# Optimization experiments

Measured on AMD Instinct MI355X. Metric: run time of the kernel, lower is better.

The kernel has to match this reference:

```python
import jax, jax.numpy as jnp
import numpy as np
import math

B, S, D = 4, 2048, 1024
NUM_HEADS = 16
HEAD_DIM = D // NUM_HEADS


def setup_inputs() -> dict:
    key = jax.random.key(0)
    ks = jax.random.split(key, 6)
    scale = 1.0 / math.sqrt(D)
    batch = jax.random.normal(ks[0], (B, S, D), dtype=jnp.float32)
    w_query = jax.random.normal(ks[1], (D, D), dtype=jnp.float32) * scale
    w_key = jax.random.normal(ks[2], (D, D), dtype=jnp.float32) * scale
    w_value = jax.random.normal(ks[3], (D, D), dtype=jnp.float32) * scale
    out_w = jax.random.normal(ks[4], (D, D), dtype=jnp.float32) * scale
    out_b = jax.random.normal(ks[5], (D,), dtype=jnp.float32) * 0.01
    return {"batch": batch, "w_query": w_query, "w_key": w_key,
            "w_value": w_value, "out_w": out_w, "out_b": out_b}


def reference(batch, w_query, w_key, w_value, out_w, out_b):
    b, s, _ = batch.shape
    # QKV projections (Linear with no bias): x @ W^T, here weights stored as [D,D] applied as x@W
    q = (batch @ w_query).reshape(b, s, NUM_HEADS, HEAD_DIM)
    k = (batch @ w_key).reshape(b, s, NUM_HEADS, HEAD_DIM)
    v = (batch @ w_value).reshape(b, s, NUM_HEADS, HEAD_DIM)
    # scores: [b, h, s, s]
    scores = jnp.einsum('bqhd,bkhd->bhqk', q, k)
    causal = jnp.tril(jnp.ones((s, s), dtype=bool))
    scores = jnp.where(causal, scores, -jnp.inf)
    # original divides by sqrt(head_dim) AFTER masking (-inf stays -inf)
    weights = jax.nn.softmax(scores / math.sqrt(HEAD_DIM), axis=-1)
    # dropout_percent = 0 -> identity
    out = jnp.einsum('bhqk,bkhd->bqhd', weights, v).reshape(b, s, D)
    return out @ out_w + out_b
```

## Files before the change

kernel.cpp:

```cpp
#include <hip/hip_runtime.h>
#include <hip/hip_bf16.h>

#define S_LEN 2048
#define D_DIM 1024
#define NHEAD 16
#define HDIM  64
#define BATCH 4
#define MROWS (BATCH*S_LEN)

typedef short bf16x8 __attribute__((ext_vector_type(8)));
typedef float f32x4  __attribute__((ext_vector_type(4)));
typedef float f32x16 __attribute__((ext_vector_type(16)));
typedef unsigned short u16;

#if __has_builtin(__builtin_amdgcn_exp2f)
#define EXP2(x) __builtin_amdgcn_exp2f(x)
#else
#define EXP2(x) __expf((x) * 0.6931471805599453f)
#endif

__device__ inline u16 f2bf(float f) {
  union { float f; unsigned u; } v; v.f = f;
  unsigned r = v.u + 0x7fff + ((v.u >> 16) & 1);
  return (u16)(r >> 16);
}

__device__ inline unsigned cvtpk(float lo, float hi_) {
  unsigned d;
  asm("v_cvt_pk_bf16_f32 %0, %1, %2" : "=v"(d) : "v"(lo), "v"(hi_));
  return d;
}

__device__ inline void perm32swap(unsigned& a, unsigned& b) {
  asm volatile("v_permlane32_swap_b32 %0, %1" : "+v"(a), "+v"(b));
}

__device__ inline void gload_lds16(const void* g, void* l) {
  __builtin_amdgcn_global_load_lds(
      (const __attribute__((address_space(1))) void*)g,
      (__attribute__((address_space(3))) void*)l, 16, 0, 0);
}

__global__ void cvt_x_kernel(const float* __restrict__ x, u16* __restrict__ xb, int n4) {
  int i = blockIdx.x * 256 + threadIdx.x;
  if (i >= n4) return;
  float4 v = reinterpret_cast<const float4*>(x)[i];
  ushort4 o;
  o.x = f2bf(v.x); o.y = f2bf(v.y); o.z = f2bf(v.z); o.w = f2bf(v.w);
  reinterpret_cast<ushort4*>(xb)[i] = o;
}

__global__ void transpose_w4_kernel(const float* __restrict__ wq, const float* __restrict__ wk,
                                    const float* __restrict__ wv, const float* __restrict__ wo,
                                    u16* __restrict__ wqkvT, u16* __restrict__ woT) {
  __shared__ float t[32][33];
  int z = blockIdx.z;
  const float* w = (z == 0) ? wq : (z == 1) ? wk : (z == 2) ? wv : wo;
  u16* wt = (z < 3) ? (wqkvT + (size_t)z * 1024 * 1024) : woT;
  int tx = threadIdx.x, ty = threadIdx.y;
  int n0 = blockIdx.x * 32, k0 = blockIdx.y * 32;
#pragma unroll
  for (int j = 0; j < 32; j += 8)
    t[ty + j][tx] = w[(size_t)(k0 + ty + j) * D_DIM + n0 + tx];
  __syncthreads();
#pragma unroll
  for (int j = 0; j < 32; j += 8)
    wt[(size_t)(n0 + ty + j) * D_DIM + k0 + tx] = f2bf(t[tx][ty + j]);
}

template <int EPI>
__global__ __launch_bounds__(256) void gemm_bt_kernel(
    const u16* __restrict__ A, const u16* __restrict__ Bt,
    void* __restrict__ Cv, u16* __restrict__ KP, u16* __restrict__ VP,
    const float* __restrict__ bias) {
  __shared__ u16 lA[128 * 32];
  __shared__ u16 lB[128 * 32];
  const int tid = threadIdx.x, wid = tid >> 6, lane = tid & 63;
  const int bm = blockIdx.y, bn = blockIdx.x;
  const int fr = lane & 15, fq = lane >> 4;
  const int r0 = wid * 32;
  const int srow = lane >> 2, scol = (lane & 3) * 8;
  const u16* gA = A + (size_t)(bm * 128 + r0 + srow) * 1024 + scol;
  const u16* gB = Bt + (size_t)(bn * 128 + r0 + srow) * 1024 + scol;
  u16* lA0 = &lA[r0 * 32];
  u16* lB0 = &lB[r0 * 32];

  f32x4 acc[4][4] = {};
  const int wm = (wid >> 1) * 64, wn = (wid & 1) * 64;

  for (int k0 = 0; k0 < 1024; k0 += 32) {
    gload_lds16(gA + k0,             lA0);
    gload_lds16(gA + k0 + 16 * 1024, lA0 + 16 * 32);
    gload_lds16(gB + k0,             lB0);
    gload_lds16(gB + k0 + 16 * 1024, lB0 + 16 * 32);
    __syncthreads();
    bf16x8 fa[4], fb[4];
#pragma unroll
    for (int i = 0; i < 4; i++) {
      fa[i] = *(const bf16x8*)&lA[(wm + i * 16 + fr) * 32 + fq * 8];
      fb[i] = *(const bf16x8*)&lB[(wn + i * 16 + fr) * 32 + fq * 8];
    }
#pragma unroll
    for (int i = 0; i < 4; i++)
#pragma unroll
      for (int j = 0; j < 4; j++)
        acc[i][j] = __builtin_amdgcn_mfma_f32_16x16x32_bf16(fa[i], fb[j], acc[i][j], 0, 0, 0);
    __syncthreads();
  }

  if (EPI == 1) {
#pragma unroll
    for (int i = 0; i < 4; i++)
#pragma unroll
      for (int j = 0; j < 4; j++)
#pragma unroll
        for (int r = 0; r < 4; r++) {
          int row = bm * 128 + wm + i * 16 + fq * 4 + r;
          int col = bn * 128 + wn + j * 16 + fr;
          ((float*)Cv)[(size_t)row * 1024 + col] = acc[i][j][r] + bias[col];
        }
    return;
  }

  const int col0 = bn * 128;
  if (col0 < 1024) {
#pragma unroll
    for (int i = 0; i < 4; i++)
#pragma unroll
      for (int j = 0; j < 4; j++)
#pragma unroll
        for (int r = 0; r < 4; r++) {
          int row = bm * 128 + wm + i * 16 + fq * 4 + r;
          int col = col0 + wn + j * 16 + fr;
          ((u16*)Cv)[(size_t)row * 1024 + col] = f2bf(acc[i][j][r]);
        }
  } else if (col0 < 2048) {
#pragma unroll
    for (int i = 0; i < 4; i++)
#pragma unroll
      for (int j = 0; j < 4; j++) {
        int col = col0 + wn + j * 16 + fr;
        int ck = col - 1024;
        int h = ck >> 6, d = ck & 63;
        int sfr = d >> 4, e = d & 7, hb = (d >> 3) & 1;
#pragma unroll
        for (int r = 0; r < 4; r++) {
          int row = bm * 128 + wm + i * 16 + fq * 4 + r;
          int b = row >> 11, sp = row & 2047;
          int bh = b * 16 + h, jt = sp >> 5;
          int lanep = (sp & 31) + 32 * hb;
          KP[((size_t)(bh * 64 + jt) * 4 + sfr) * 512 + lanep * 8 + e] = f2bf(acc[i][j][r]);
        }
      }
  } else {
#pragma unroll
    for (int i = 0; i < 4; i++)
#pragma unroll
      for (int j = 0; j < 4; j++) {
        int col = col0 + wn + j * 16 + fr;
        int cv = col - 2048;
        int h = cv >> 6, d = cv & 63;
        int R0 = bm * 128 + wm + i * 16 + fq * 4;
        int b = R0 >> 11, sp0 = R0 & 2047;
        int bh = b * 16 + h, jt = sp0 >> 5;
        int c = (d >> 5) * 2 + ((sp0 >> 4) & 1);
        int lanep = (d & 31) + 32 * ((sp0 >> 3) & 1);
        int e0 = sp0 & 7;
        ushort4 ov;
        ov.x = f2bf(acc[i][j][0]); ov.y = f2bf(acc[i][j][1]);
        ov.z = f2bf(acc[i][j][2]); ov.w = f2bf(acc[i][j][3]);
        *(ushort4*)(VP + ((size_t)(bh * 64 + jt) * 4 + c) * 512 + lanep * 8 + e0) = ov;
      }
  }
}

__global__ __launch_bounds__(256) void attn_kernel(
    const u16* __restrict__ Q, const u16* __restrict__ KP,
    const u16* __restrict__ VP, u16* __restrict__ O) {
  const int tid = threadIdx.x, wid = tid >> 6, lane = tid & 63;
  const int lq = lane & 31, hi = lane >> 5;
  int f = blockIdx.x;
  int xcd = f & 7, kk = f >> 3;
  int bh = xcd * 8 + (kk & 7);
  int qblk = 15 - (kk >> 3);
  int b = bh >> 4, h = bh & 15;
  int q0 = qblk * 128 + wid * 32;
  int q = q0 + lq;

  const u16* Qrow = Q + (size_t)(b * S_LEN + q) * D_DIM + h * HDIM;
  bf16x8 qf[4];
#pragma unroll
  for (int s = 0; s < 4; s++)
    qf[s] = *(const bf16x8*)(Qrow + s * 16 + hi * 8);

  const bf16x8* KPt = (const bf16x8*)KP + (size_t)bh * 64 * 4 * 64;
  const bf16x8* VPt = (const bf16x8*)VP + (size_t)bh * 64 * 4 * 64;

  f32x16 acc0 = {}, acc1 = {};
  float m = -3.0e38f, l = 0.f;
  const int nt = qblk * 4 + wid + 1;

  for (int t = 0; t < nt; ++t) {
    const int j0 = t * 32;
    const size_t fb = (size_t)t * 4 * 64 + lane;
    bf16x8 kf0 = KPt[fb], kf1 = KPt[fb + 64], kf2 = KPt[fb + 128], kf3 = KPt[fb + 192];
    bf16x8 vf00 = VPt[fb], vf01 = VPt[fb + 64], vf10 = VPt[fb + 128], vf11 = VPt[fb + 192];

    f32x16 sa = {};
    __builtin_amdgcn_s_setprio(1);
    sa = __builtin_amdgcn_mfma_f32_32x32x16_bf16(kf0, qf[0], sa, 0, 0, 0);
    sa = __builtin_amdgcn_mfma_f32_32x32x16_bf16(kf1, qf[1], sa, 0, 0, 0);
    sa = __builtin_amdgcn_mfma_f32_32x32x16_bf16(kf2, qf[2], sa, 0, 0, 0);
    sa = __builtin_amdgcn_mfma_f32_32x32x16_bf16(kf3, qf[3], sa, 0, 0, 0);
    __builtin_amdgcn_s_setprio(0);

    float p[16];
#pragma unroll
    for (int r = 0; r < 16; ++r) p[r] = sa[r] * 0.1803368801f;

    if (t == nt - 1) {
#pragma unroll
      for (int r = 0; r < 16; ++r) {
        int kidx = j0 + (r & 3) + 8 * (r >> 2) + 4 * hi;
        if (kidx > q) p[r] = -3.0e38f;
      }
    }

    float x8[8], x4[4], x2[2];
#pragma unroll
    for (int i = 0; i < 8; ++i) x8[i] = fmaxf(p[2 * i], p[2 * i + 1]);
#pragma unroll
    for (int i = 0; i < 4; ++i) x4[i] = fmaxf(x8[2 * i], x8[2 * i + 1]);
    x2[0] = fmaxf(x4[0], x4[1]); x2[1] = fmaxf(x4[2], x4[3]);
    float pm = fmaxf(x2[0], x2[1]);
    pm = fmaxf(pm, __shfl_xor(pm, 32));

    if (__any(pm > m + 11.5f)) {
      float mn = fmaxf(m, pm);
      float sc = EXP2(m - mn);
      l *= sc;
#pragma unroll
      for (int r = 0; r < 16; ++r) { acc0[r] *= sc; acc1[r] *= sc; }
      m = mn;
    }

    float rs = 0.f;
#pragma unroll
    for (int r = 0; r < 16; ++r) { p[r] = EXP2(p[r] - m); rs += p[r]; }
    rs += __shfl_xor(rs, 32);
    l += rs;

    unsigned c0 = cvtpk(p[0],  p[1]),  c1 = cvtpk(p[2],  p[3]);
    unsigned c2 = cvtpk(p[4],  p[5]),  c3 = cvtpk(p[6],  p[7]);
    unsigned c4 = cvtpk(p[8],  p[9]),  c5 = cvtpk(p[10], p[11]);
    unsigned c6 = cvtpk(p[12], p[13]), c7 = cvtpk(p[14], p[15]);
    perm32swap(c0, c2); perm32swap(c1, c3);
    perm32swap(c4, c6); perm32swap(c5, c7);
    union U4 { unsigned u[4]; bf16x8 v; } F0, F1;
    F0.u[0] = c0; F0.u[1] = c1; F0.u[2] = c2; F0.u[3] = c3;
    F1.u[0] = c4; F1.u[1] = c5; F1.u[2] = c6; F1.u[3] = c7;

    __builtin_amdgcn_s_setprio(1);
    acc0 = __builtin_amdgcn_mfma_f32_32x32x16_bf16(vf00, F0.v, acc0, 0, 0, 0);
    acc0 = __builtin_amdgcn_mfma_f32_32x32x16_bf16(vf01, F1.v, acc0, 0, 0, 0);
    acc1 = __builtin_amdgcn_mfma_f32_32x32x16_bf16(vf10, F0.v, acc1, 0, 0, 0);
    acc1 = __builtin_amdgcn_mfma_f32_32x32x16_bf16(vf11, F1.v, acc1, 0, 0, 0);
    __builtin_amdgcn_s_setprio(0);
  }

  float inv = 1.f / l;
  u16* Orow = O + (size_t)(b * S_LEN + q) * D_DIM + h * HDIM;
#pragma unroll
  for (int g = 0; g < 4; ++g) {
    ushort4 o4;
    o4.x = f2bf(acc0[g * 4 + 0] * inv);
    o4.y = f2bf(acc0[g * 4 + 1] * inv);
    o4.z = f2bf(acc0[g * 4 + 2] * inv);
    o4.w = f2bf(acc0[g * 4 + 3] * inv);
    *(ushort4*)(Orow + 8 * g + 4 * hi) = o4;
  }
#pragma unroll
  for (int g = 0; g < 4; ++g) {
    ushort4 o4;
    o4.x = f2bf(acc1[g * 4 + 0] * inv);
    o4.y = f2bf(acc1[g * 4 + 1] * inv);
    o4.z = f2bf(acc1[g * 4 + 2] * inv);
    o4.w = f2bf(acc1[g * 4 + 3] * inv);
    *(ushort4*)(Orow + 32 + 8 * g + 4 * hi) = o4;
  }
}

extern "C" void kernel_launch(void* const* d_in, const int* in_sizes, int n_in,
                              void* d_out, int out_size, void* d_ws, size_t ws_size,
                              hipStream_t stream) {
  const float* x  = (const float*)d_in[0];
  const float* wq = (const float*)d_in[1];
  const float* wk = (const float*)d_in[2];
  const float* wv = (const float*)d_in[3];
  const float* wo = (const float*)d_in[4];
  const float* ob = (const float*)d_in[5];
  float* out = (float*)d_out;

  char* ws = (char*)d_ws;
  u16* Xb    = (u16*)(ws);
  u16* Ab    = (u16*)(ws);
  u16* Qb    = (u16*)(ws + (size_t)16 * 1024 * 1024);
  u16* KPb   = (u16*)(ws + (size_t)32 * 1024 * 1024);
  u16* VPb   = (u16*)(ws + (size_t)48 * 1024 * 1024);
  u16* WqkvT = (u16*)(ws + (size_t)64 * 1024 * 1024);
  u16* WoT   = (u16*)(ws + (size_t)70 * 1024 * 1024);

  cvt_x_kernel<<<(MROWS * D_DIM / 4) / 256, 256, 0, stream>>>(x, Xb, MROWS * D_DIM / 4);

  transpose_w4_kernel<<<dim3(32, 32, 4), dim3(32, 8), 0, stream>>>(
      wq, wk, wv, wo, WqkvT, WoT);

  gemm_bt_kernel<0><<<dim3(24, 64), 256, 0, stream>>>(
      Xb, WqkvT, Qb, KPb, VPb, nullptr);

  attn_kernel<<<dim3(1024), 256, 0, stream>>>(Qb, KPb, VPb, Ab);

  gemm_bt_kernel<1><<<dim3(8, 64), 256, 0, stream>>>(
      Ab, WoT, out, nullptr, nullptr, ob);
}
```

Baseline: 177.6 us.

## Double-buffer LDS tiles in the projection GEMM to overlap loads with MFMA

The GEMM mainloop now keeps two LDS buffers for A and B. The global-to-LDS loads for the next K tile are issued before the MFMAs on the current tile, so memory latency can overlap with compute, and each iteration uses one barrier instead of two. The cost is twice the LDS per block, which may lower occupancy, and the loop is now fully unrolled. The manual s_waitcnt and s_barrier depend on the compiler not reordering the LDS reads.

```diff
diff --git a/kernel.cpp b/kernel.cpp
--- a/kernel.cpp
+++ b/kernel.cpp
@@ -18,6 +18,9 @@
 #else
 #define EXP2(x) __expf((x) * 0.6931471805599453f)
 #endif
+
+#define BAR() asm volatile("s_barrier" ::: "memory")
+#define WAITV0() asm volatile("s_waitcnt vmcnt(0)" ::: "memory")
 
 __device__ inline u16 f2bf(float f) {
   union { float f; unsigned u; } v; v.f = f;
@@ -73,8 +76,8 @@
     const u16* __restrict__ A, const u16* __restrict__ Bt,
     void* __restrict__ Cv, u16* __restrict__ KP, u16* __restrict__ VP,
     const float* __restrict__ bias) {
-  __shared__ u16 lA[128 * 32];
-  __shared__ u16 lB[128 * 32];
+  __shared__ u16 lA[2][128 * 32];
+  __shared__ u16 lB[2][128 * 32];
   const int tid = threadIdx.x, wid = tid >> 6, lane = tid & 63;
   const int bm = blockIdx.y, bn = blockIdx.x;
   const int fr = lane & 15, fq = lane >> 4;
@@ -82,30 +85,39 @@
   const int srow = lane >> 2, scol = (lane & 3) * 8;
   const u16* gA = A + (size_t)(bm * 128 + r0 + srow) * 1024 + scol;
   const u16* gB = Bt + (size_t)(bn * 128 + r0 + srow) * 1024 + scol;
-  u16* lA0 = &lA[r0 * 32];
-  u16* lB0 = &lB[r0 * 32];
 
   f32x4 acc[4][4] = {};
   const int wm = (wid >> 1) * 64, wn = (wid & 1) * 64;
 
+  gload_lds16(gA,             &lA[0][r0 * 32]);
+  gload_lds16(gA + 16 * 1024, &lA[0][r0 * 32 + 16 * 32]);
+  gload_lds16(gB,             &lB[0][r0 * 32]);
+  gload_lds16(gB + 16 * 1024, &lB[0][r0 * 32 + 16 * 32]);
+  WAITV0();
+  BAR();
+
+#pragma unroll
   for (int k0 = 0; k0 < 1024; k0 += 32) {
-    gload_lds16(gA + k0,             lA0);
-    gload_lds16(gA + k0 + 16 * 1024, lA0 + 16 * 32);
-    gload_lds16(gB + k0,             lB0);
-    gload_lds16(gB + k0 + 16 * 1024, lB0 + 16 * 32);
-    __syncthreads();
+    const int cur = (k0 >> 5) & 1, nxt = cur ^ 1;
+    if (k0 + 32 < 1024) {
+      gload_lds16(gA + k0 + 32,             &lA[nxt][r0 * 32]);
+      gload_lds16(gA + k0 + 32 + 16 * 1024, &lA[nxt][r0 * 32 + 16 * 32]);
+      gload_lds16(gB + k0 + 32,             &lB[nxt][r0 * 32]);
+      gload_lds16(gB + k0 + 32 + 16 * 1024, &lB[nxt][r0 * 32 + 16 * 32]);
+    }
     bf16x8 fa[4], fb[4];
 #pragma unroll
     for (int i = 0; i < 4; i++) {
-      fa[i] = *(const bf16x8*)&lA[(wm + i * 16 + fr) * 32 + fq * 8];
-      fb[i] = *(const bf16x8*)&lB[(wn + i * 16 + fr) * 32 + fq * 8];
+      fa[i] = *(const bf16x8*)&lA[cur][(wm + i * 16 + fr) * 32 + fq * 8];
+      fb[i] = *(const bf16x8*)&lB[cur][(wn + i * 16 + fr) * 32 + fq * 8];
     }
 #pragma unroll
     for (int i = 0; i < 4; i++)
 #pragma unroll
       for (int j = 0; j < 4; j++)
         acc[i][j] = __builtin_amdgcn_mfma_f32_16x16x32_bf16(fa[i], fb[j], acc[i][j], 0, 0, 0);
-    __syncthreads();
+    WAITV0();
+    BAR();
   }
 
   if (EPI == 1) {
```

Result: faster. 172.8 us (-2.7%).
